# Performance work log

Hardware: AMD Instinct MI355X
Metric: run time of the kernel (lower is better)

## Reference

```python
import jax, jax.numpy as jnp
import numpy as np

L, H, NH, HD, FF = 4, 1024, 16, 64, 4096
EPS = 1e-5
NEG = jnp.finfo(jnp.float32).min


def _ln(x, g, b):
    m = x.mean(-1, keepdims=True)
    v = ((x - m) ** 2).mean(-1, keepdims=True)
    return (x - m) * jax.lax.rsqrt(v + EPS) * g + b


def _rotate_half(x):
    # interleaved: out[...,0::2] = -x[...,1::2]; out[...,1::2] = x[...,0::2]
    x1 = x[..., ::2]
    x2 = x[..., 1::2]
    return jnp.stack((-x2, x1), axis=-1).reshape(x.shape)


def _rope_cos_sin(position_ids):
    # position_ids: [B,S] int -> cos/sin [B,S,1,HD] (freqs repeated interleaved)
    inv_freq = 1.0 / (10000.0 ** (jnp.arange(0, HD, 2, dtype=jnp.float32) / HD))
    freqs = position_ids.astype(jnp.float32)[..., None] * inv_freq  # [B,S,HD/2]
    emb = jnp.repeat(freqs, 2, axis=-1)  # [B,S,HD]
    return jnp.cos(emb)[:, :, None, :], jnp.sin(emb)[:, :, None, :]


def _apply_rope(x, cos, sin):
    return x * cos + _rotate_half(x) * sin


def setup_inputs() -> dict:
    key = jax.random.key(0)
    ks = jax.random.split(key, 8)
    s = 0.02
    inp = {
        "inputs_embeds": jax.random.normal(ks[0], (4, 1024, H), jnp.float32),
        "attention_mask": jnp.ones((4, 1024), dtype=bool),
        "Wqkv": jax.random.normal(ks[1], (L, H, 3 * H), jnp.float32) * s,
        "bqkv": jnp.zeros((L, 3 * H), jnp.float32),
        "Wo": jax.random.normal(ks[2], (L, H, H), jnp.float32) * s,
        "bo": jnp.zeros((L, H), jnp.float32),
        "ln1_g": jnp.ones((L, H), jnp.float32),
        "ln1_b": jnp.zeros((L, H), jnp.float32),
        "ln2_g": jnp.ones((L, H), jnp.float32),
        "ln2_b": jnp.zeros((L, H), jnp.float32),
        "Wfc": jax.random.normal(ks[3], (L, H, FF), jnp.float32) * s,
        "bfc": jnp.zeros((L, FF), jnp.float32),
        "Wproj": jax.random.normal(ks[4], (L, FF, H), jnp.float32) * s,
        "bproj": jnp.zeros((L, H), jnp.float32),
        "lnf_g": jnp.ones((H,), jnp.float32),
        "lnf_b": jnp.zeros((H,), jnp.float32),
    }
    return inp


def reference(inputs_embeds, attention_mask, Wqkv, bqkv, Wo, bo, ln1_g, ln1_b,
              ln2_g, ln2_b, Wfc, bfc, Wproj, bproj, lnf_g, lnf_b):
    B, S, _ = inputs_embeds.shape
    mask = attention_mask  # bool [B,S]
    maskf = mask.astype(inputs_embeds.dtype)[:, :, None]  # [B,S,1]

    # position ids from mask (cumsum - 1, clamped to 0 on pad)
    pid = jnp.cumsum(mask.astype(jnp.int32), axis=-1) - 1
    pid = jnp.where(mask, pid, 0)
    cos, sin = _rope_cos_sin(pid)

    # causal + padding mask: [B,1,S,S]
    qpos = jnp.arange(S)
    causal = (qpos[None, :] <= qpos[:, None])[None, None]  # [1,1,S,S]
    amask = causal & mask[:, None, None, :]

    scale = 1.0 / (HD ** 0.5)
    h = inputs_embeds * maskf  # drop() is identity in eval

    for l in range(L):
        hs = _ln(h, ln1_g[l], ln1_b[l])
        qkv = hs @ Wqkv[l] + bqkv[l]
        q, k, v = jnp.split(qkv, 3, axis=-1)
        q = _apply_rope(q.reshape(B, S, NH, HD), cos, sin)
        k = _apply_rope(k.reshape(B, S, NH, HD), cos, sin)
        v = v.reshape(B, S, NH, HD)
        scores = jnp.einsum("bqhd,bkhd->bhqk", q, k) * scale
        scores = jnp.where(amask, scores, NEG)
        probs = jax.nn.softmax(scores, axis=-1)
        attn = jnp.einsum("bhqk,bkhd->bqhd", probs, v).reshape(B, S, H)
        attn = attn @ Wo[l] + bo[l]
        h = h + attn
        m = _ln(h, ln2_g[l], ln2_b[l])
        m = jax.nn.gelu(m @ Wfc[l] + bfc[l], approximate=True) @ Wproj[l] + bproj[l]
        h = (h + m) * maskf

    h = _ln(h, lnf_g, lnf_b) * maskf
    return h
```

## Files before the change

### kernel.cpp

```cpp
#include <hip/hip_runtime.h>
#include <math.h>


typedef unsigned short u16;
typedef unsigned int u32;
typedef __attribute__((ext_vector_type(8))) short short8;
typedef __attribute__((ext_vector_type(4))) float f32x4;
typedef __attribute__((ext_vector_type(4))) u16 u16x4;

#define NEGV (-3.402823466e38f)

__device__ __forceinline__ u16 f2bf(float f) {
  union { float f; u32 u; } v; v.f = f;
  u32 r = v.u + 0x7FFFu + ((v.u >> 16) & 1u);
  return (u16)(r >> 16);
}

__device__ __forceinline__ float gelu_tanh(float x) {
  float z = 0.7978845608028654f * (x + 0.044715f * x * x * x);
  z = fmaxf(fminf(z, 30.f), -30.f);
  float t = __expf(2.f * z);
  return 0.5f * x * (1.f + (t - 1.f) / (t + 1.f));
}

__global__ __launch_bounds__(1024) void mask_pid_kernel(const void* __restrict__ maskp,
                                                        float* __restrict__ maskf,
                                                        int* __restrict__ pid) {
  int b = blockIdx.x, s = threadIdx.x;
  const u32* wp = (const u32*)maskp;
  bool int_mode = ((wp[0] & 0xFFFFFF00u) == 0u);
  int mv;
  if (int_mode) mv = (((const int*)maskp)[b * 1024 + s] != 0) ? 1 : 0;
  else          mv = (((const unsigned char*)maskp)[b * 1024 + s] != 0) ? 1 : 0;
  __shared__ int sc[1024];
  sc[s] = mv;
  __syncthreads();
  for (int off = 1; off < 1024; off <<= 1) {
    int add = (s >= off) ? sc[s - off] : 0;
    __syncthreads();
    sc[s] += add;
    __syncthreads();
  }
  pid[b * 1024 + s] = mv ? (sc[s] - 1) : 0;
  maskf[b * 1024 + s] = (float)mv;
}

__global__ __launch_bounds__(256) void embed_kernel(const float* __restrict__ e,
                                                    const float* __restrict__ maskf,
                                                    float* __restrict__ h) {
  int idx = blockIdx.x * 256 + threadIdx.x;
  size_t o = (size_t)idx * 4;
  int row = (int)(o >> 10);
  float mf = maskf[row];
  float4 v = *(const float4*)(e + o);
  float4 r; r.x = v.x * mf; r.y = v.y * mf; r.z = v.z * mf; r.w = v.w * mf;
  *(float4*)(h + o) = r;
}

__global__ __launch_bounds__(256) void transpose_bf16(const float* __restrict__ in,
                                                      u16* __restrict__ out,
                                                      int K, int N) {
  __shared__ float t[32][33];
  int tx = threadIdx.x, ty = threadIdx.y;
  int n0 = blockIdx.x * 32, k0 = blockIdx.y * 32;
#pragma unroll
  for (int j = 0; j < 4; ++j) {
    int k = ty + j * 8;
    t[k][tx] = in[(size_t)(k0 + k) * N + n0 + tx];
  }
  __syncthreads();
#pragma unroll
  for (int j = 0; j < 4; ++j) {
    int n = ty + j * 8;
    out[(size_t)(n0 + n) * K + k0 + tx] = f2bf(t[tx][n]);
  }
}

template <int MODE>
__global__ __launch_bounds__(256) void ln_kernel(const float* __restrict__ x,
                                                 const float* __restrict__ g,
                                                 const float* __restrict__ bb,
                                                 u16* __restrict__ yb,
                                                 float* __restrict__ yf,
                                                 const float* __restrict__ maskf) {
  int row = blockIdx.x, tid = threadIdx.x;
  const float* xr = x + (size_t)row * 1024;
  float4 v = *(const float4*)(xr + tid * 4);
  float s = v.x + v.y + v.z + v.w;
  float q = v.x * v.x + v.y * v.y + v.z * v.z + v.w * v.w;
#pragma unroll
  for (int off = 32; off >= 1; off >>= 1) {
    s += __shfl_xor(s, off);
    q += __shfl_xor(q, off);
  }
  __shared__ float ps[4], pq[4];
  int w = tid >> 6, lane = tid & 63;
  if (lane == 0) { ps[w] = s; pq[w] = q; }
  __syncthreads();
  float S = ps[0] + ps[1] + ps[2] + ps[3];
  float Q = pq[0] + pq[1] + pq[2] + pq[3];
  float mean = S * (1.f / 1024.f);
  float var = fmaxf(Q * (1.f / 1024.f) - mean * mean, 0.f);
  float rstd = rsqrtf(var + 1e-5f);
  int c = tid * 4;
  float4 gv = *(const float4*)(g + c);
  float4 bv = *(const float4*)(bb + c);
  float y0 = (v.x - mean) * rstd * gv.x + bv.x;
  float y1 = (v.y - mean) * rstd * gv.y + bv.y;
  float y2 = (v.z - mean) * rstd * gv.z + bv.z;
  float y3 = (v.w - mean) * rstd * gv.w + bv.w;
  if (MODE == 0) {
    u16x4 o; o.x = f2bf(y0); o.y = f2bf(y1); o.z = f2bf(y2); o.w = f2bf(y3);
    *(u16x4*)(yb + (size_t)row * 1024 + c) = o;
  } else {
    float mf = maskf[row];
    float4 o; o.x = y0 * mf; o.y = y1 * mf; o.z = y2 * mf; o.w = y3 * mf;
    *(float4*)(yf + (size_t)row * 1024 + c) = o;
  }
}

template <int EPI>
__global__ __launch_bounds__(256) void gemm_bf16(const u16* __restrict__ A,
                                                 const u16* __restrict__ Bt,
                                                 const float* __restrict__ bias,
                                                 float* __restrict__ Of,
                                                 u16* __restrict__ Ob,
                                                 const float* __restrict__ maskf,
                                                 int M, int N, int K) {
  __shared__ __align__(16) u16 As[64][40];
  __shared__ __align__(16) u16 Bs[64][40];
  const int tid = threadIdx.x;
  const int lane = tid & 63, w = tid >> 6;
  const int wm = w >> 1, wn = w & 1;
  const int m0 = blockIdx.y * 64, n0 = blockIdx.x * 64;
  const int lm = lane & 15, lq = lane >> 4;

  f32x4 acc[2][2] = {};
  const int r = tid >> 2;
  const int cg = (tid & 3) * 8;
  const u16* Ap = A + (size_t)(m0 + r) * K + cg;
  const u16* Bp = Bt + (size_t)(n0 + r) * K + cg;

  for (int k0 = 0; k0 < K; k0 += 32) {
    uint4 av = *(const uint4*)(Ap + k0);
    uint4 bv = *(const uint4*)(Bp + k0);
    *(uint4*)(&As[r][cg]) = av;
    *(uint4*)(&Bs[r][cg]) = bv;
    __syncthreads();
    short8 af[2], bf[2];
    af[0] = *(const short8*)(&As[wm * 32 + lm][lq * 8]);
    af[1] = *(const short8*)(&As[wm * 32 + 16 + lm][lq * 8]);
    bf[0] = *(const short8*)(&Bs[wn * 32 + lm][lq * 8]);
    bf[1] = *(const short8*)(&Bs[wn * 32 + 16 + lm][lq * 8]);
#pragma unroll
    for (int mt = 0; mt < 2; ++mt)
#pragma unroll
      for (int nt = 0; nt < 2; ++nt)
        acc[mt][nt] = __builtin_amdgcn_mfma_f32_16x16x32_bf16(af[mt], bf[nt], acc[mt][nt], 0, 0, 0);
    __syncthreads();
  }

#pragma unroll
  for (int mt = 0; mt < 2; ++mt) {
#pragma unroll
    for (int nt = 0; nt < 2; ++nt) {
      int col = n0 + wn * 32 + nt * 16 + lm;
      float bvv = bias[col];
#pragma unroll
      for (int rr = 0; rr < 4; ++rr) {
        int row = m0 + wm * 32 + mt * 16 + lq * 4 + rr;
        size_t idx = (size_t)row * N + col;
        float v = acc[mt][nt][rr] + bvv;
        if (EPI == 0) {
          Of[idx] = v;
        } else if (EPI == 1) {
          Of[idx] += v;
        } else if (EPI == 2) {
          Ob[idx] = f2bf(gelu_tanh(v));
        } else {
          Of[idx] = (Of[idx] + v) * maskf[row];
        }
      }
    }
  }
}

__global__ __launch_bounds__(256) void rope_kernel(const float* __restrict__ qkv,
                                                   const int* __restrict__ pid,
                                                   u16* __restrict__ qh,
                                                   u16* __restrict__ kh,
                                                   u16* __restrict__ vh) {
  int idx = blockIdx.x * 256 + threadIdx.x;
  int i = idx & 31;
  int hh = (idx >> 5) & 15;
  int row = idx >> 9;
  int b = row >> 10, s = row & 1023;
  float p = (float)pid[row];
  float inv = __expf(-(float)(2 * i) * (9.210340371976184f / 64.f));
  float th = p * inv;
  float c = cosf(th), sn = sinf(th);
  size_t base = (size_t)row * 3072 + hh * 64 + 2 * i;
  float q0 = qkv[base], q1 = qkv[base + 1];
  float k0 = qkv[base + 1024], k1 = qkv[base + 1025];
  float v0 = qkv[base + 2048], v1 = qkv[base + 2049];
  float qr0 = (q0 * c - q1 * sn) * 0.125f;
  float qr1 = (q1 * c + q0 * sn) * 0.125f;
  float kr0 = k0 * c - k1 * sn;
  float kr1 = k1 * c + k0 * sn;
  size_t hbase = ((size_t)(b * 16 + hh) * 1024 + s) * 64 + 2 * i;
  *(u32*)(qh + hbase) = (u32)f2bf(qr0) | ((u32)f2bf(qr1) << 16);
  *(u32*)(kh + hbase) = (u32)f2bf(kr0) | ((u32)f2bf(kr1) << 16);
  *(u32*)(vh + hbase) = (u32)f2bf(v0) | ((u32)f2bf(v1) << 16);
}

__global__ __launch_bounds__(256) void attn_mfma(const u16* __restrict__ qh,
                                                 const u16* __restrict__ kh,
                                                 const u16* __restrict__ vh,
                                                 const float* __restrict__ maskf,
                                                 u16* __restrict__ ctx) {
  const int b = blockIdx.z, h = blockIdx.y, qt = blockIdx.x;
  const int tid = threadIdx.x, lane = tid & 63, w = tid >> 6;
  const int ln = lane & 15, kg = lane >> 4;
  const int q0 = qt * 64;
  const size_t hb = (size_t)(b * 16 + h) * 1024 * 64;

  __shared__ __align__(16) u16 Ks[64][72];
  __shared__ __align__(16) u16 VsT[64][72];
  __shared__ __align__(16) u16 Ps[64][72];
  __shared__ float Ms[64];

  const int qrow = q0 + w * 16 + ln;
  short8 qa0 = *(const short8*)(qh + hb + (size_t)qrow * 64 + kg * 8);
  short8 qa1 = *(const short8*)(qh + hb + (size_t)qrow * 64 + 32 + kg * 8);

  f32x4 Oc[4] = {};
  float m_i[4], l_i[4];
#pragma unroll
  for (int r = 0; r < 4; ++r) { m_i[r] = NEGV; l_i[r] = 0.f; }

  const int ntiles = qt + 1;
  for (int t = 0; t < ntiles; ++t) {
    __syncthreads();
    {
      int row = tid >> 2, c8 = (tid & 3) * 8;
      const u16* kp2 = kh + hb + (size_t)(t * 64 + row) * 64;
      *(uint4*)(&Ks[row][c8]) = *(const uint4*)(kp2 + c8);
      *(uint4*)(&Ks[row][c8 + 32]) = *(const uint4*)(kp2 + c8 + 32);
    }
    {
      int kp = tid >> 3, dg = tid & 7;
      const u16* vp0 = vh + hb + (size_t)(t * 64 + 2 * kp) * 64 + dg * 8;
      uint4 r0 = *(const uint4*)vp0;
      uint4 r1 = *(const uint4*)(vp0 + 64);
      u32 a0[4] = {r0.x, r0.y, r0.z, r0.w};
      u32 a1[4] = {r1.x, r1.y, r1.z, r1.w};
#pragma unroll
      for (int j = 0; j < 8; ++j) {
        u32 lo = (a0[j >> 1] >> (16 * (j & 1))) & 0xffffu;
        u32 hi = (a1[j >> 1] >> (16 * (j & 1))) & 0xffffu;
        *(u32*)(&VsT[dg * 8 + j][2 * kp]) = lo | (hi << 16);
      }
    }
    if (tid < 64) Ms[tid] = maskf[b * 1024 + t * 64 + tid];
    __syncthreads();

    f32x4 Sc[4];
#pragma unroll
    for (int c = 0; c < 4; ++c) {
      short8 kb0 = *(const short8*)(&Ks[c * 16 + ln][kg * 8]);
      short8 kb1 = *(const short8*)(&Ks[c * 16 + ln][32 + kg * 8]);
      f32x4 z = {};
      z = __builtin_amdgcn_mfma_f32_16x16x32_bf16(qa0, kb0, z, 0, 0, 0);
      Sc[c] = __builtin_amdgcn_mfma_f32_16x16x32_bf16(qa1, kb1, Sc[c] = z, 0, 0, 0);
    }
    float mk[4];
#pragma unroll
    for (int c = 0; c < 4; ++c) mk[c] = Ms[c * 16 + ln];

#pragma unroll
    for (int r = 0; r < 4; ++r) {
      int qg = q0 + w * 16 + kg * 4 + r;
      float vmax = NEGV;
#pragma unroll
      for (int c = 0; c < 4; ++c) {
        int key = t * 64 + c * 16 + ln;
        bool valid = (key <= qg) && (mk[c] != 0.f);
        float sv = valid ? Sc[c][r] : NEGV;
        Sc[c][r] = sv;
        vmax = fmaxf(vmax, sv);
      }
#pragma unroll
      for (int off = 1; off <= 8; off <<= 1) vmax = fmaxf(vmax, __shfl_xor(vmax, off));
      float mnew = fmaxf(m_i[r], vmax);
      float alpha = __expf(m_i[r] - mnew);
      m_i[r] = mnew;
      float ls = 0.f;
#pragma unroll
      for (int c = 0; c < 4; ++c) {
        float p = __expf(Sc[c][r] - mnew);
        Sc[c][r] = p;
        ls += p;
      }
#pragma unroll
      for (int off = 1; off <= 8; off <<= 1) ls += __shfl_xor(ls, off);
      l_i[r] = l_i[r] * alpha + ls;
#pragma unroll
      for (int c = 0; c < 4; ++c) Oc[c][r] *= alpha;
#pragma unroll
      for (int c = 0; c < 4; ++c) Ps[w * 16 + kg * 4 + r][c * 16 + ln] = f2bf(Sc[c][r]);
    }
    __syncthreads();

    short8 pa0 = *(const short8*)(&Ps[w * 16 + ln][kg * 8]);
    short8 pa1 = *(const short8*)(&Ps[w * 16 + ln][32 + kg * 8]);
#pragma unroll
    for (int c = 0; c < 4; ++c) {
      short8 vb0 = *(const short8*)(&VsT[c * 16 + ln][kg * 8]);
      short8 vb1 = *(const short8*)(&VsT[c * 16 + ln][32 + kg * 8]);
      Oc[c] = __builtin_amdgcn_mfma_f32_16x16x32_bf16(pa0, vb0, Oc[c], 0, 0, 0);
      Oc[c] = __builtin_amdgcn_mfma_f32_16x16x32_bf16(pa1, vb1, Oc[c], 0, 0, 0);
    }
  }

#pragma unroll
  for (int r = 0; r < 4; ++r) {
    float rl = 1.f / l_i[r];
    int row = q0 + w * 16 + kg * 4 + r;
#pragma unroll
    for (int c = 0; c < 4; ++c) {
      ctx[(size_t)(b * 1024 + row) * 1024 + h * 64 + c * 16 + ln] = f2bf(Oc[c][r] * rl);
    }
  }
}

extern "C" void kernel_launch(void* const* d_in, const int* in_sizes, int n_in,
                              void* d_out, int out_size, void* d_ws, size_t ws_size,
                              hipStream_t stream) {
  const float* embeds = (const float*)d_in[0];
  const void* amask   = d_in[1];
  const float* Wqkv = (const float*)d_in[2];
  const float* bqkv = (const float*)d_in[3];
  const float* Wo   = (const float*)d_in[4];
  const float* bo   = (const float*)d_in[5];
  const float* ln1g = (const float*)d_in[6];
  const float* ln1b = (const float*)d_in[7];
  const float* ln2g = (const float*)d_in[8];
  const float* ln2b = (const float*)d_in[9];
  const float* Wfc  = (const float*)d_in[10];
  const float* bfc  = (const float*)d_in[11];
  const float* Wpj  = (const float*)d_in[12];
  const float* bpj  = (const float*)d_in[13];
  const float* lnfg = (const float*)d_in[14];
  const float* lnfb = (const float*)d_in[15];
  float* out = (float*)d_out;

  char* ws = (char*)d_ws;
  float* h     = (float*)(ws);
  float* qkv   = (float*)(ws + (size_t)(16u << 20));
  u16*   xb    = (u16*)(ws + (size_t)(64u << 20));
  u16*   ffb   = (u16*)(ws + (size_t)(72u << 20));
  u16*   qhp   = (u16*)(ws + (size_t)(72u << 20));
  u16*   khp   = (u16*)(ws + (size_t)(80u << 20));
  u16*   vhp   = (u16*)(ws + (size_t)(88u << 20));
  u16*   wqT   = (u16*)(ws + (size_t)(104u << 20));
  u16*   woT   = (u16*)(ws + (size_t)(110u << 20));
  u16*   wfT   = (u16*)(ws + (size_t)(112u << 20));
  u16*   wpT   = (u16*)(ws + (size_t)(120u << 20));
  float* maskf = (float*)(ws + (size_t)(128u << 20));
  int*   pid   = (int*)(ws + (size_t)(128u << 20) + (16u << 10));

  mask_pid_kernel<<<4, 1024, 0, stream>>>(amask, maskf, pid);
  embed_kernel<<<4096, 256, 0, stream>>>(embeds, maskf, h);

  for (int l = 0; l < 4; ++l) {
    transpose_bf16<<<dim3(96, 32), dim3(32, 8), 0, stream>>>(Wqkv + (size_t)l * 1024 * 3072, wqT, 1024, 3072);
    transpose_bf16<<<dim3(32, 32), dim3(32, 8), 0, stream>>>(Wo + (size_t)l * 1024 * 1024, woT, 1024, 1024);
    transpose_bf16<<<dim3(128, 32), dim3(32, 8), 0, stream>>>(Wfc + (size_t)l * 1024 * 4096, wfT, 1024, 4096);
    transpose_bf16<<<dim3(32, 128), dim3(32, 8), 0, stream>>>(Wpj + (size_t)l * 4096 * 1024, wpT, 4096, 1024);

    ln_kernel<0><<<4096, 256, 0, stream>>>(h, ln1g + l * 1024, ln1b + l * 1024, xb, nullptr, nullptr);
    gemm_bf16<0><<<dim3(48, 64), 256, 0, stream>>>(xb, wqT, bqkv + l * 3072, qkv, nullptr, nullptr, 4096, 3072, 1024);
    rope_kernel<<<8192, 256, 0, stream>>>(qkv, pid, qhp, khp, vhp);
    attn_mfma<<<dim3(16, 16, 4), 256, 0, stream>>>(qhp, khp, vhp, maskf, xb);
    gemm_bf16<1><<<dim3(16, 64), 256, 0, stream>>>(xb, woT, bo + l * 1024, h, nullptr, nullptr, 4096, 1024, 1024);
    ln_kernel<0><<<4096, 256, 0, stream>>>(h, ln2g + l * 1024, ln2b + l * 1024, xb, nullptr, nullptr);
    gemm_bf16<2><<<dim3(64, 64), 256, 0, stream>>>(xb, wfT, bfc + l * 4096, nullptr, ffb, nullptr, 4096, 4096, 1024);
    gemm_bf16<3><<<dim3(16, 64), 256, 0, stream>>>(ffb, wpT, bpj + l * 1024, h, nullptr, maskf, 4096, 1024, 4096);
  }
  ln_kernel<1><<<4096, 256, 0, stream>>>(h, lnfg, lnfb, nullptr, out, maskf);
}
```

Baseline: 1.671 ms.

## Enlarge GEMM tiles to 128x128 and load tiles via direct global-to-LDS

Replaces the 64x64 GEMM with a 128x128 block tile in which each wave computes a 64x64 sub-tile of 4x4 MFMA fragments, and fills shared memory with global_load_lds instead of going through registers. The larger tile raises operand reuse per LDS load and halves global traffic per output. The direct LDS loads drop the register staging step. LDS rows are now unpadded (stride 32), which may cause bank conflicts on fragment reads. Grid sizes shrink, which lowers occupancy, and accumulator register pressure rises.

After: 1.598 ms. 4.4% less time.

```diff
diff --git a/kernel.cpp b/kernel.cpp
--- a/kernel.cpp
+++ b/kernel.cpp
@@ -21,6 +21,11 @@
   z = fmaxf(fminf(z, 30.f), -30.f);
   float t = __expf(2.f * z);
   return 0.5f * x * (1.f + (t - 1.f) / (t + 1.f));
+}
+
+__device__ __forceinline__ void gld_lds16(const u16* g, u16* l) {
+  __builtin_amdgcn_global_load_lds((const __attribute__((address_space(1))) u32*)g,
+                                   (__attribute__((address_space(3))) u32*)l, 16, 0, 0);
 }
 
 __global__ __launch_bounds__(1024) void mask_pid_kernel(const void* __restrict__ maskp,
@@ -120,55 +125,64 @@
 }
 
 template <int EPI>
-__global__ __launch_bounds__(256) void gemm_bf16(const u16* __restrict__ A,
-                                                 const u16* __restrict__ Bt,
-                                                 const float* __restrict__ bias,
-                                                 float* __restrict__ Of,
-                                                 u16* __restrict__ Ob,
-                                                 const float* __restrict__ maskf,
-                                                 int M, int N, int K) {
-  __shared__ __align__(16) u16 As[64][40];
-  __shared__ __align__(16) u16 Bs[64][40];
+__global__ __launch_bounds__(256) void gemm128(const u16* __restrict__ A,
+                                               const u16* __restrict__ Bt,
+                                               const float* __restrict__ bias,
+                                               float* __restrict__ Of,
+                                               u16* __restrict__ Ob,
+                                               const float* __restrict__ maskf,
+                                               int M, int N, int K) {
+  __shared__ __align__(16) u16 As[128 * 32];
+  __shared__ __align__(16) u16 Bs[128 * 32];
   const int tid = threadIdx.x;
   const int lane = tid & 63, w = tid >> 6;
   const int wm = w >> 1, wn = w & 1;
-  const int m0 = blockIdx.y * 64, n0 = blockIdx.x * 64;
-  const int lm = lane & 15, lq = lane >> 4;
-
-  f32x4 acc[2][2] = {};
-  const int r = tid >> 2;
-  const int cg = (tid & 3) * 8;
-  const u16* Ap = A + (size_t)(m0 + r) * K + cg;
-  const u16* Bp = Bt + (size_t)(n0 + r) * K + cg;
+  const int m0 = blockIdx.y * 128, n0 = blockIdx.x * 128;
+  const int ln = lane & 15, kg = lane >> 4;
+
+  f32x4 acc[4][4] = {};
+
+  const int r0 = tid >> 2, g0 = (tid & 3) * 8;
+  const u16* Ap0 = A + (size_t)(m0 + r0) * K + g0;
+  const u16* Ap1 = A + (size_t)(m0 + 64 + r0) * K + g0;
+  const u16* Bp0 = Bt + (size_t)(n0 + r0) * K + g0;
+  const u16* Bp1 = Bt + (size_t)(n0 + 64 + r0) * K + g0;
+  u16* AsD0 = As + tid * 8;
+  u16* AsD1 = As + (tid + 256) * 8;
+  u16* BsD0 = Bs + tid * 8;
+  u16* BsD1 = Bs + (tid + 256) * 8;
 
   for (int k0 = 0; k0 < K; k0 += 32) {
-    uint4 av = *(const uint4*)(Ap + k0);
-    uint4 bv = *(const uint4*)(Bp + k0);
-    *(uint4*)(&As[r][cg]) = av;
-    *(uint4*)(&Bs[r][cg]) = bv;
-    __syncthreads();
-    short8 af[2], bf[2];
-    af[0] = *(const short8*)(&As[wm * 32 + lm][lq * 8]);
-    af[1] = *(const short8*)(&As[wm * 32 + 16 + lm][lq * 8]);
-    bf[0] = *(const short8*)(&Bs[wn * 32 + lm][lq * 8]);
-    bf[1] = *(const short8*)(&Bs[wn * 32 + 16 + lm][lq * 8]);
-#pragma unroll
-    for (int mt = 0; mt < 2; ++mt)
-#pragma unroll
-      for (int nt = 0; nt < 2; ++nt)
-        acc[mt][nt] = __builtin_amdgcn_mfma_f32_16x16x32_bf16(af[mt], bf[nt], acc[mt][nt], 0, 0, 0);
-    __syncthreads();
-  }
-
-#pragma unroll
-  for (int mt = 0; mt < 2; ++mt) {
-#pragma unroll
-    for (int nt = 0; nt < 2; ++nt) {
-      int col = n0 + wn * 32 + nt * 16 + lm;
+    __syncthreads();
+    gld_lds16(Ap0 + k0, AsD0);
+    gld_lds16(Ap1 + k0, AsD1);
+    gld_lds16(Bp0 + k0, BsD0);
+    gld_lds16(Bp1 + k0, BsD1);
+    __syncthreads();
+
+    short8 af[4], bfr[4];
+#pragma unroll
+    for (int mt = 0; mt < 4; ++mt)
+      af[mt] = *(const short8*)(As + (wm * 64 + mt * 16 + ln) * 32 + kg * 8);
+#pragma unroll
+    for (int nt = 0; nt < 4; ++nt)
+      bfr[nt] = *(const short8*)(Bs + (wn * 64 + nt * 16 + ln) * 32 + kg * 8);
+#pragma unroll
+    for (int mt = 0; mt < 4; ++mt)
+#pragma unroll
+      for (int nt = 0; nt < 4; ++nt)
+        acc[mt][nt] = __builtin_amdgcn_mfma_f32_16x16x32_bf16(af[mt], bfr[nt], acc[mt][nt], 0, 0, 0);
+  }
+
+#pragma unroll
+  for (int mt = 0; mt < 4; ++mt) {
+#pragma unroll
+    for (int nt = 0; nt < 4; ++nt) {
+      int col = n0 + wn * 64 + nt * 16 + ln;
       float bvv = bias[col];
 #pragma unroll
       for (int rr = 0; rr < 4; ++rr) {
-        int row = m0 + wm * 32 + mt * 16 + lq * 4 + rr;
+        int row = m0 + wm * 64 + mt * 16 + kg * 4 + rr;
         size_t idx = (size_t)row * N + col;
         float v = acc[mt][nt][rr] + bvv;
         if (EPI == 0) {
@@ -271,7 +285,7 @@
       short8 kb1 = *(const short8*)(&Ks[c * 16 + ln][32 + kg * 8]);
       f32x4 z = {};
       z = __builtin_amdgcn_mfma_f32_16x16x32_bf16(qa0, kb0, z, 0, 0, 0);
-      Sc[c] = __builtin_amdgcn_mfma_f32_16x16x32_bf16(qa1, kb1, Sc[c] = z, 0, 0, 0);
+      Sc[c] = __builtin_amdgcn_mfma_f32_16x16x32_bf16(qa1, kb1, z, 0, 0, 0);
     }
     float mk[4];
 #pragma unroll
@@ -379,13 +393,13 @@
     transpose_bf16<<<dim3(32, 128), dim3(32, 8), 0, stream>>>(Wpj + (size_t)l * 4096 * 1024, wpT, 4096, 1024);
 
     ln_kernel<0><<<4096, 256, 0, stream>>>(h, ln1g + l * 1024, ln1b + l * 1024, xb, nullptr, nullptr);
-    gemm_bf16<0><<<dim3(48, 64), 256, 0, stream>>>(xb, wqT, bqkv + l * 3072, qkv, nullptr, nullptr, 4096, 3072, 1024);
+    gemm128<0><<<dim3(24, 32), 256, 0, stream>>>(xb, wqT, bqkv + l * 3072, qkv, nullptr, nullptr, 4096, 3072, 1024);
     rope_kernel<<<8192, 256, 0, stream>>>(qkv, pid, qhp, khp, vhp);
     attn_mfma<<<dim3(16, 16, 4), 256, 0, stream>>>(qhp, khp, vhp, maskf, xb);
-    gemm_bf16<1><<<dim3(16, 64), 256, 0, stream>>>(xb, woT, bo + l * 1024, h, nullptr, nullptr, 4096, 1024, 1024);
+    gemm128<1><<<dim3(8, 32), 256, 0, stream>>>(xb, woT, bo + l * 1024, h, nullptr, nullptr, 4096, 1024, 1024);
     ln_kernel<0><<<4096, 256, 0, stream>>>(h, ln2g + l * 1024, ln2b + l * 1024, xb, nullptr, nullptr);
-    gemm_bf16<2><<<dim3(64, 64), 256, 0, stream>>>(xb, wfT, bfc + l * 4096, nullptr, ffb, nullptr, 4096, 4096, 1024);
-    gemm_bf16<3><<<dim3(16, 64), 256, 0, stream>>>(ffb, wpT, bpj + l * 1024, h, nullptr, maskf, 4096, 1024, 4096);
+    gemm128<2><<<dim3(32, 32), 256, 0, stream>>>(xb, wfT, bfc + l * 4096, nullptr, ffb, nullptr, 4096, 4096, 1024);
+    gemm128<3><<<dim3(8, 32), 256, 0, stream>>>(ffb, wpT, bpj + l * 1024, h, nullptr, maskf, 4096, 1024, 4096);
   }
   ln_kernel<1><<<4096, 256, 0, stream>>>(h, lnfg, lnfb, nullptr, out, maskf);
 }
```
